# Performance work log

Measured on AMD Instinct MI355X. Metric: run time of the kernel, lower is better.

The kernel has to match this reference:

```python
import jax, jax.numpy as jnp
import numpy as np

NUM_HEAD = 16


def setup_inputs() -> dict:
    key = jax.random.key(0)
    k1, k2, k3 = jax.random.split(key, 3)
    E = 1024
    x = jax.random.normal(k1, (4, 2048, E), dtype=jnp.float32)
    W1 = jax.random.normal(k2, (E, 3 * E), dtype=jnp.float32) * 0.02
    b1 = jnp.zeros((3 * E,), dtype=jnp.float32)
    W2 = jax.random.normal(k3, (E, E), dtype=jnp.float32) * 0.02
    b2 = jnp.zeros((E,), dtype=jnp.float32)
    return {"x": x, "W1": W1, "b1": b1, "W2": W2, "b2": b2}


def reference(x, W1, b1, W2, b2):
    # Fused QKV projection: (n, s, 3E)
    h = x @ W1 + b1
    n, s, _ = h.shape
    # Split into heads FIRST (matches torch reshape), then transpose: (n, H, s, 3*d_head)
    h = h.reshape(n, s, NUM_HEAD, -1).transpose(0, 2, 1, 3)
    # Chunk last dim into q, k, v: each (n, H, s, d_head)
    q, k, v = jnp.split(h, 3, axis=-1)
    dk = jnp.asarray(v.shape[-1], x.dtype) ** 0.5
    # Naive full S x S attention (faithful to source)
    w = jnp.einsum("nhqd,nhkd->nhqk", q, k) / dk
    w = jax.nn.softmax(w, axis=-1)  # dropout1 is identity at eval
    att = jnp.einsum("nhqk,nhkd->nhqd", w, v)
    att = att.transpose(0, 2, 1, 3).reshape(n, s, -1)  # (n, s, E)
    return att @ W2 + b2  # dropout2 identity at eval
```

## Files before the change

kernel.cpp:

```cpp
#include <hip/hip_runtime.h>
#include <math.h>
#include <stdint.h>
#include <stddef.h>


#define SEQ    2048
#define NB     4
#define E_DIM  1024
#define N1     3072
#define M_TOK  8192
#define NHEAD  16
#define DHEAD  64

typedef __attribute__((ext_vector_type(4))) float    floatx4;
typedef __attribute__((ext_vector_type(8))) short    shortx8;
typedef __attribute__((ext_vector_type(4))) unsigned short ushortx4;

__device__ __forceinline__ unsigned short f2bf(float f) {
    union { float f; unsigned u; } v; v.f = f;
    unsigned r = (v.u + 0x7FFFu + ((v.u >> 16) & 1u)) >> 16;
    return (unsigned short)r;
}
__device__ __forceinline__ unsigned fbits(float f) {
    union { float f; unsigned u; } v; v.f = f; return v.u;
}
__device__ __forceinline__ float bitsf(unsigned u) {
    union { unsigned u; float f; } v; v.u = u; return v.f;
}

__device__ __forceinline__ void gl_lds16(const void* g, void* l) {
    __builtin_amdgcn_global_load_lds(
        (const __attribute__((address_space(1))) unsigned int*)g,
        (__attribute__((address_space(3))) unsigned int*)l, 16, 0, 0);
}

__global__ __launch_bounds__(256) void cvt_bf16(
    const float* __restrict__ in, unsigned short* __restrict__ out)
{
    const size_t i = ((size_t)blockIdx.x * 256 + threadIdx.x) * 8;
    float4 a = *(const float4*)(in + i);
    float4 b = *(const float4*)(in + i + 4);
    ushortx4 o0 = { f2bf(a.x), f2bf(a.y), f2bf(a.z), f2bf(a.w) };
    ushortx4 o1 = { f2bf(b.x), f2bf(b.y), f2bf(b.z), f2bf(b.w) };
    *(ushortx4*)(out + i)     = o0;
    *(ushortx4*)(out + i + 4) = o1;
}

__global__ __launch_bounds__(256) void cvt_transpose(
    const float* __restrict__ W, unsigned short* __restrict__ Wt, int K, int N)
{
    __shared__ unsigned short tile[32][33];
    const int tx = threadIdx.x, ty = threadIdx.y;
    const int n0 = blockIdx.x * 32, k0 = blockIdx.y * 32;
#pragma unroll
    for (int r = 0; r < 4; ++r) {
        const int k = ty + r * 8;
        tile[tx][k] = f2bf(W[(size_t)(k0 + k) * N + n0 + tx]);
    }
    __syncthreads();
#pragma unroll
    for (int r = 0; r < 4; ++r) {
        const int n = ty + r * 8;
        Wt[(size_t)(n0 + n) * K + k0 + tx] = tile[n][tx];
    }
}

__global__ __launch_bounds__(256) void vtrans(
    const unsigned short* __restrict__ h, unsigned short* __restrict__ Vt)
{
    __shared__ unsigned short tile[64][68];
    const int t  = threadIdx.x;
    const int bh = blockIdx.y, n = bh >> 4, head = bh & 15;
    const int s0 = blockIdx.x * 64;
    const unsigned short* hV = h + (size_t)n * SEQ * N1 + head * (3 * DHEAD) + 2 * DHEAD;

#pragma unroll
    for (int rr = 0; rr < 4; ++rr) {
        const int s  = rr * 16 + (t >> 4);
        const int d4 = (t & 15) * 4;
        ushortx4 v = *(const ushortx4*)(hV + (size_t)(s0 + s) * N1 + d4);
        tile[d4 + 0][s] = v.x;
        tile[d4 + 1][s] = v.y;
        tile[d4 + 2][s] = v.z;
        tile[d4 + 3][s] = v.w;
    }
    __syncthreads();
    unsigned short* Vb = Vt + (size_t)bh * DHEAD * SEQ;
#pragma unroll
    for (int rr = 0; rr < 4; ++rr) {
        const int d  = rr * 16 + (t >> 4);
        const int s4 = (t & 15) * 4;
        ushortx4 o = { tile[d][s4], tile[d][s4 + 1], tile[d][s4 + 2], tile[d][s4 + 3] };
        *(ushortx4*)(Vb + (size_t)d * SEQ + s0 + s4) = o;
    }
}

template <bool OUT_BF16>
__global__ __launch_bounds__(256) void gemm_bf16(
    const short* __restrict__ A, const short* __restrict__ Bt,
    const float* __restrict__ bias, void* __restrict__ Cout,
    int M, int N, int K)
{
    __shared__ short As[128 * 32];
    __shared__ short Bs[128 * 32];

    const int t    = threadIdx.x;
    const int lane = t & 63, w = t >> 6;
    const int quad = lane >> 4, l15 = lane & 15;
    const int bm = blockIdx.y * 128, bn = blockIdx.x * 128;
    const int m0w = (w >> 1) * 64, n0w = (w & 1) * 64;

    const int lrow = lane >> 2;
    const int lcol = (lane & 3) * 8;
    const short* Ag0 = A  + (size_t)(bm + (2 * w + 0) * 16 + lrow) * K + lcol;
    const short* Ag1 = A  + (size_t)(bm + (2 * w + 1) * 16 + lrow) * K + lcol;
    const short* Bg0 = Bt + (size_t)(bn + (2 * w + 0) * 16 + lrow) * K + lcol;
    const short* Bg1 = Bt + (size_t)(bn + (2 * w + 1) * 16 + lrow) * K + lcol;
    short* Al0 = As + (2 * w + 0) * 512;
    short* Al1 = As + (2 * w + 1) * 512;
    short* Bl0 = Bs + (2 * w + 0) * 512;
    short* Bl1 = Bs + (2 * w + 1) * 512;

    floatx4 acc[4][4];
#pragma unroll
    for (int i = 0; i < 4; ++i)
#pragma unroll
        for (int j = 0; j < 4; ++j) acc[i][j] = (floatx4)0.f;

    for (int k0 = 0; k0 < K; k0 += 32) {
        __syncthreads();
        gl_lds16(Ag0, Al0); gl_lds16(Ag1, Al1);
        gl_lds16(Bg0, Bl0); gl_lds16(Bg1, Bl1);
        Ag0 += 32; Ag1 += 32; Bg0 += 32; Bg1 += 32;
        __syncthreads();

        shortx8 af[4], bf[4];
#pragma unroll
        for (int mi = 0; mi < 4; ++mi)
            af[mi] = *(const shortx8*)(As + (m0w + mi * 16 + l15) * 32 + quad * 8);
#pragma unroll
        for (int ni = 0; ni < 4; ++ni)
            bf[ni] = *(const shortx8*)(Bs + (n0w + ni * 16 + l15) * 32 + quad * 8);
#pragma unroll
        for (int mi = 0; mi < 4; ++mi)
#pragma unroll
            for (int ni = 0; ni < 4; ++ni)
                acc[mi][ni] = __builtin_amdgcn_mfma_f32_16x16x32_bf16(
                    af[mi], bf[ni], acc[mi][ni], 0, 0, 0);
    }

    float bv[4];
#pragma unroll
    for (int ni = 0; ni < 4; ++ni) bv[ni] = bias[bn + n0w + ni * 16 + l15];

#pragma unroll
    for (int mi = 0; mi < 4; ++mi)
#pragma unroll
        for (int ni = 0; ni < 4; ++ni)
#pragma unroll
            for (int r = 0; r < 4; ++r) {
                const size_t row = bm + m0w + mi * 16 + quad * 4 + r;
                const size_t col = bn + n0w + ni * 16 + l15;
                const float  val = acc[mi][ni][r] + bv[ni];
                if (OUT_BF16)
                    ((unsigned short*)Cout)[row * N + col] = f2bf(val);
                else
                    ((float*)Cout)[row * N + col] = val;
            }
}

__global__ __launch_bounds__(256, 2) void attn_mfma(
    const short* __restrict__ h, const short* __restrict__ Vt,
    unsigned short* __restrict__ att)
{
    __shared__ short Ks[64 * 72];
    __shared__ short Vs[64 * 72];
    __shared__ short Pl[4][64 * 72];
    __shared__ float Ls[4][64];

    const int t    = threadIdx.x;
    const int lane = t & 63, w = t >> 6;
    const int quad = lane >> 4, l15 = lane & 15;
    const int bh = blockIdx.x, n = bh >> 4, head = bh & 15;
    const int q0 = blockIdx.y * 256 + w * 64;

    const short* hQ  = h + (size_t)n * SEQ * N1 + head * (3 * DHEAD);
    const short* hK  = hQ + DHEAD;
    const short* Vtb = Vt + (size_t)bh * DHEAD * SEQ;

    const int srow = t >> 2;
    const int scol = (t & 3) * 16;
    const short* gK = hK  + (size_t)srow * N1  + scol;
    const short* gV = Vtb + (size_t)srow * SEQ + scol;
    short* lK = Ks + srow * 72 + scol;
    short* lV = Vs + srow * 72 + scol;

    shortx8 qf[4][2];
#pragma unroll
    for (int qt = 0; qt < 4; ++qt)
#pragma unroll
        for (int kt = 0; kt < 2; ++kt)
            qf[qt][kt] = *(const shortx8*)(hQ + (size_t)(q0 + qt * 16 + l15) * N1
                                           + kt * 32 + quad * 8);

    floatx4 O[4][4];
    float lsum[4];
#pragma unroll
    for (int mi = 0; mi < 4; ++mi) {
        lsum[mi] = 0.f;
#pragma unroll
        for (int nt = 0; nt < 4; ++nt) O[mi][nt] = (floatx4)0.f;
    }

    int4 ka = *(const int4*)gK, kb = *(const int4*)(gK + 8);
    int4 va = *(const int4*)gV, vb = *(const int4*)(gV + 8);

    const float SC = 0.18033688f;
    short* Pw = Pl[w];

    for (int kv0 = 0; kv0 < SEQ; kv0 += 64) {
        __syncthreads();
        *(int4*)lK       = ka;
        *(int4*)(lK + 8) = kb;
        *(int4*)lV       = va;
        *(int4*)(lV + 8) = vb;
        __syncthreads();
        if (kv0 + 64 < SEQ) {
            const short* gKn = gK + (size_t)(kv0 + 64) * N1;
            const short* gVn = gV + (kv0 + 64);
            ka = *(const int4*)gKn; kb = *(const int4*)(gKn + 8);
            va = *(const int4*)gVn; vb = *(const int4*)(gVn + 8);
        }

#pragma unroll
        for (int kvt = 0; kvt < 4; ++kvt) {
            shortx8 kf0 = *(const shortx8*)(Ks + (kvt * 16 + l15) * 72 + quad * 8);
            shortx8 kf1 = *(const shortx8*)(Ks + (kvt * 16 + l15) * 72 + 32 + quad * 8);
            floatx4 s[4];
#pragma unroll
            for (int qt = 0; qt < 4; ++qt) {
                s[qt] = __builtin_amdgcn_mfma_f32_16x16x32_bf16(
                    kf0, qf[qt][0], (floatx4)0.f, 0, 0, 0);
                s[qt] = __builtin_amdgcn_mfma_f32_16x16x32_bf16(
                    kf1, qf[qt][1], s[qt], 0, 0, 0);
            }
#pragma unroll
            for (int qt = 0; qt < 4; ++qt) {
                const float p0 = exp2f(s[qt][0] * SC);
                const float p1 = exp2f(s[qt][1] * SC);
                const float p2 = exp2f(s[qt][2] * SC);
                const float p3 = exp2f(s[qt][3] * SC);
                const unsigned d01 = __builtin_amdgcn_perm(fbits(p1), fbits(p0), 0x07060302u);
                const unsigned d23 = __builtin_amdgcn_perm(fbits(p3), fbits(p2), 0x07060302u);
                lsum[qt] += bitsf(d01 << 16) + bitsf(d01 & 0xFFFF0000u)
                          + bitsf(d23 << 16) + bitsf(d23 & 0xFFFF0000u);
                uint2 pk = { d01, d23 };
                *(uint2*)(Pw + (qt * 16 + l15) * 72 + kvt * 16 + quad * 4) = pk;
            }
        }

#pragma unroll
        for (int kt2 = 0; kt2 < 2; ++kt2) {
            shortx8 pf[4], vf[4];
#pragma unroll
            for (int mi = 0; mi < 4; ++mi)
                pf[mi] = *(const shortx8*)(Pw + (mi * 16 + l15) * 72 + kt2 * 32 + quad * 8);
#pragma unroll
            for (int nt = 0; nt < 4; ++nt)
                vf[nt] = *(const shortx8*)(Vs + (nt * 16 + l15) * 72 + kt2 * 32 + quad * 8);
#pragma unroll
            for (int mi = 0; mi < 4; ++mi)
#pragma unroll
                for (int nt = 0; nt < 4; ++nt)
                    O[mi][nt] = __builtin_amdgcn_mfma_f32_16x16x32_bf16(
                        pf[mi], vf[nt], O[mi][nt], 0, 0, 0);
        }
    }

#pragma unroll
    for (int qt = 0; qt < 4; ++qt) {
        lsum[qt] += __shfl_xor(lsum[qt], 16);
        lsum[qt] += __shfl_xor(lsum[qt], 32);
    }
    if (quad == 0) {
#pragma unroll
        for (int qt = 0; qt < 4; ++qt) Ls[w][qt * 16 + l15] = lsum[qt];
    }

#pragma unroll
    for (int mi = 0; mi < 4; ++mi)
#pragma unroll
        for (int r = 0; r < 4; ++r) {
            const int   ql  = mi * 16 + quad * 4 + r;
            const float inv = 1.f / Ls[w][ql];
            const size_t row = (size_t)n * SEQ + q0 + ql;
#pragma unroll
            for (int nt = 0; nt < 4; ++nt)
                att[row * E_DIM + head * DHEAD + nt * 16 + l15] =
                    f2bf(O[mi][nt][r] * inv);
        }
}

extern "C" void kernel_launch(void* const* d_in, const int* in_sizes, int n_in,
                              void* d_out, int out_size, void* d_ws, size_t ws_size,
                              hipStream_t stream)
{
    const float* x  = (const float*)d_in[0];
    const float* W1 = (const float*)d_in[1];
    const float* b1 = (const float*)d_in[2];
    const float* W2 = (const float*)d_in[3];
    const float* b2 = (const float*)d_in[4];
    float* out = (float*)d_out;

    char* ws = (char*)d_ws;
    unsigned short* x_bf  = (unsigned short*)(ws);
    unsigned short* W1t   = (unsigned short*)(ws + (16u << 20));
    unsigned short* W2t   = (unsigned short*)(ws + (22u << 20));
    unsigned short* h_bf  = (unsigned short*)(ws + (24u << 20));
    unsigned short* attb  = (unsigned short*)(ws + (72u << 20));
    unsigned short* Vtw   = (unsigned short*)(ws + (88u << 20));

    cvt_bf16<<<dim3((M_TOK * E_DIM) / (256 * 8)), 256, 0, stream>>>(x, x_bf);
    cvt_transpose<<<dim3(N1 / 32, E_DIM / 32), dim3(32, 8), 0, stream>>>(W1, W1t, E_DIM, N1);
    cvt_transpose<<<dim3(E_DIM / 32, E_DIM / 32), dim3(32, 8), 0, stream>>>(W2, W2t, E_DIM, E_DIM);

    gemm_bf16<true><<<dim3(N1 / 128, M_TOK / 128), 256, 0, stream>>>(
        (const short*)x_bf, (const short*)W1t, b1, h_bf, M_TOK, N1, E_DIM);

    vtrans<<<dim3(SEQ / 64, NB * NHEAD), 256, 0, stream>>>(h_bf, Vtw);

    attn_mfma<<<dim3(NB * NHEAD, SEQ / 256), 256, 0, stream>>>(
        (const short*)h_bf, (const short*)Vtw, attb);

    gemm_bf16<false><<<dim3(E_DIM / 128, M_TOK / 128), 256, 0, stream>>>(
        (const short*)attb, (const short*)W2t, b2, out, M_TOK, E_DIM, E_DIM);
}
```

Before: 327.1 us.

## Fuse V transpose into QKV GEMM epilogue, swizzle attention LDS, prescale Q

```diff
diff --git a/kernel.cpp b/kernel.cpp
--- a/kernel.cpp
+++ b/kernel.cpp
@@ -65,40 +65,11 @@
     }
 }
 
-__global__ __launch_bounds__(256) void vtrans(
-    const unsigned short* __restrict__ h, unsigned short* __restrict__ Vt)
-{
-    __shared__ unsigned short tile[64][68];
-    const int t  = threadIdx.x;
-    const int bh = blockIdx.y, n = bh >> 4, head = bh & 15;
-    const int s0 = blockIdx.x * 64;
-    const unsigned short* hV = h + (size_t)n * SEQ * N1 + head * (3 * DHEAD) + 2 * DHEAD;
-
-#pragma unroll
-    for (int rr = 0; rr < 4; ++rr) {
-        const int s  = rr * 16 + (t >> 4);
-        const int d4 = (t & 15) * 4;
-        ushortx4 v = *(const ushortx4*)(hV + (size_t)(s0 + s) * N1 + d4);
-        tile[d4 + 0][s] = v.x;
-        tile[d4 + 1][s] = v.y;
-        tile[d4 + 2][s] = v.z;
-        tile[d4 + 3][s] = v.w;
-    }
-    __syncthreads();
-    unsigned short* Vb = Vt + (size_t)bh * DHEAD * SEQ;
-#pragma unroll
-    for (int rr = 0; rr < 4; ++rr) {
-        const int d  = rr * 16 + (t >> 4);
-        const int s4 = (t & 15) * 4;
-        ushortx4 o = { tile[d][s4], tile[d][s4 + 1], tile[d][s4 + 2], tile[d][s4 + 3] };
-        *(ushortx4*)(Vb + (size_t)d * SEQ + s0 + s4) = o;
-    }
-}
-
-template <bool OUT_BF16>
+template <bool OUT_BF16, bool FUSE>
 __global__ __launch_bounds__(256) void gemm_bf16(
     const short* __restrict__ A, const short* __restrict__ Bt,
     const float* __restrict__ bias, void* __restrict__ Cout,
+    unsigned short* __restrict__ Vt,
     int M, int N, int K)
 {
     __shared__ short As[128 * 32];
@@ -154,33 +125,55 @@
     for (int ni = 0; ni < 4; ++ni) bv[ni] = bias[bn + n0w + ni * 16 + l15];
 
 #pragma unroll
-    for (int mi = 0; mi < 4; ++mi)
-#pragma unroll
-        for (int ni = 0; ni < 4; ++ni)
-#pragma unroll
-            for (int r = 0; r < 4; ++r) {
-                const size_t row = bm + m0w + mi * 16 + quad * 4 + r;
-                const size_t col = bn + n0w + ni * 16 + l15;
-                const float  val = acc[mi][ni][r] + bv[ni];
-                if (OUT_BF16)
-                    ((unsigned short*)Cout)[row * N + col] = f2bf(val);
-                else
-                    ((float*)Cout)[row * N + col] = val;
+    for (int ni = 0; ni < 4; ++ni) {
+        const int col   = bn + n0w + ni * 16 + l15;
+        const int cm    = col % 192;
+        const int vhead = col / 192;
+#pragma unroll
+        for (int mi = 0; mi < 4; ++mi) {
+            const int row0 = bm + m0w + mi * 16 + quad * 4;
+            float v[4];
+#pragma unroll
+            for (int r = 0; r < 4; ++r) v[r] = acc[mi][ni][r] + bv[ni];
+            if (OUT_BF16) {
+                if (FUSE && cm < DHEAD) {
+#pragma unroll
+                    for (int r = 0; r < 4; ++r) v[r] *= 0.125f;
+                }
+                unsigned short* H = (unsigned short*)Cout;
+#pragma unroll
+                for (int r = 0; r < 4; ++r)
+                    H[(size_t)(row0 + r) * N + col] = f2bf(v[r]);
+                if (FUSE && cm >= 2 * DHEAD) {
+                    const int nb = row0 >> 11;
+                    const int s  = row0 & 2047;
+                    const int d  = cm - 2 * DHEAD;
+                    ushortx4 pk = { f2bf(v[0]), f2bf(v[1]), f2bf(v[2]), f2bf(v[3]) };
+                    *(ushortx4*)(Vt + ((size_t)(nb * NHEAD + vhead) * DHEAD + d) * SEQ + s) = pk;
+                }
+            } else {
+                float* C = (float*)Cout;
+#pragma unroll
+                for (int r = 0; r < 4; ++r)
+                    C[(size_t)(row0 + r) * N + col] = v[r];
             }
-}
-
-__global__ __launch_bounds__(256, 2) void attn_mfma(
+        }
+    }
+}
+
+__global__ __launch_bounds__(256, 3) void attn_mfma(
     const short* __restrict__ h, const short* __restrict__ Vt,
     unsigned short* __restrict__ att)
 {
-    __shared__ short Ks[64 * 72];
-    __shared__ short Vs[64 * 72];
-    __shared__ short Pl[4][64 * 72];
+    __shared__ short Ks[64 * 64];
+    __shared__ short Vs[64 * 64];
+    __shared__ short Pl[4][64 * 64];
     __shared__ float Ls[4][64];
 
     const int t    = threadIdx.x;
     const int lane = t & 63, w = t >> 6;
     const int quad = lane >> 4, l15 = lane & 15;
+    const int r7   = l15 & 7;
     const int bh = blockIdx.x, n = bh >> 4, head = bh & 15;
     const int q0 = blockIdx.y * 256 + w * 64;
 
@@ -189,11 +182,14 @@
     const short* Vtb = Vt + (size_t)bh * DHEAD * SEQ;
 
     const int srow = t >> 2;
-    const int scol = (t & 3) * 16;
-    const short* gK = hK  + (size_t)srow * N1  + scol;
-    const short* gV = Vtb + (size_t)srow * SEQ + scol;
-    short* lK = Ks + srow * 72 + scol;
-    short* lV = Vs + srow * 72 + scol;
+    const int sc0  = (t & 3) * 2;
+    const int sk   = srow & 7;
+    const short* gK = hK  + (size_t)srow * N1  + sc0 * 8;
+    const short* gV = Vtb + (size_t)srow * SEQ + sc0 * 8;
+    short* lK0 = Ks + srow * 64 + ((sc0    ) ^ sk) * 8;
+    short* lK1 = Ks + srow * 64 + ((sc0 + 1) ^ sk) * 8;
+    short* lV0 = Vs + srow * 64 + ((sc0    ) ^ sk) * 8;
+    short* lV1 = Vs + srow * 64 + ((sc0 + 1) ^ sk) * 8;
 
     shortx8 qf[4][2];
 #pragma unroll
@@ -215,15 +211,14 @@
     int4 ka = *(const int4*)gK, kb = *(const int4*)(gK + 8);
     int4 va = *(const int4*)gV, vb = *(const int4*)(gV + 8);
 
-    const float SC = 0.18033688f;
     short* Pw = Pl[w];
 
     for (int kv0 = 0; kv0 < SEQ; kv0 += 64) {
         __syncthreads();
-        *(int4*)lK       = ka;
-        *(int4*)(lK + 8) = kb;
-        *(int4*)lV       = va;
-        *(int4*)(lV + 8) = vb;
+        *(int4*)lK0 = ka;
+        *(int4*)lK1 = kb;
+        *(int4*)lV0 = va;
+        *(int4*)lV1 = vb;
         __syncthreads();
         if (kv0 + 64 < SEQ) {
             const short* gKn = gK + (size_t)(kv0 + 64) * N1;
@@ -234,8 +229,9 @@
 
 #pragma unroll
         for (int kvt = 0; kvt < 4; ++kvt) {
-            shortx8 kf0 = *(const shortx8*)(Ks + (kvt * 16 + l15) * 72 + quad * 8);
-            shortx8 kf1 = *(const shortx8*)(Ks + (kvt * 16 + l15) * 72 + 32 + quad * 8);
+            const short* krow = Ks + (kvt * 16 + l15) * 64;
+            shortx8 kf0 = *(const shortx8*)(krow + ((quad ^ r7) * 8));
+            shortx8 kf1 = *(const shortx8*)(krow + (((quad ^ r7) ^ 4) * 8));
             floatx4 s[4];
 #pragma unroll
             for (int qt = 0; qt < 4; ++qt) {
@@ -246,28 +242,31 @@
             }
 #pragma unroll
             for (int qt = 0; qt < 4; ++qt) {
-                const float p0 = exp2f(s[qt][0] * SC);
-                const float p1 = exp2f(s[qt][1] * SC);
-                const float p2 = exp2f(s[qt][2] * SC);
-                const float p3 = exp2f(s[qt][3] * SC);
+                const float p0 = __expf(s[qt][0]);
+                const float p1 = __expf(s[qt][1]);
+                const float p2 = __expf(s[qt][2]);
+                const float p3 = __expf(s[qt][3]);
                 const unsigned d01 = __builtin_amdgcn_perm(fbits(p1), fbits(p0), 0x07060302u);
                 const unsigned d23 = __builtin_amdgcn_perm(fbits(p3), fbits(p2), 0x07060302u);
                 lsum[qt] += bitsf(d01 << 16) + bitsf(d01 & 0xFFFF0000u)
                           + bitsf(d23 << 16) + bitsf(d23 & 0xFFFF0000u);
                 uint2 pk = { d01, d23 };
-                *(uint2*)(Pw + (qt * 16 + l15) * 72 + kvt * 16 + quad * 4) = pk;
+                *(uint2*)(Pw + (qt * 16 + l15) * 64
+                          + ((2 * kvt + (quad >> 1)) ^ r7) * 8 + (quad & 1) * 4) = pk;
             }
         }
 
 #pragma unroll
         for (int kt2 = 0; kt2 < 2; ++kt2) {
+            const int coff = (((kt2 * 4 + quad) ^ r7)) * 8;
             shortx8 pf[4], vf[4];
 #pragma unroll
             for (int mi = 0; mi < 4; ++mi)
-                pf[mi] = *(const shortx8*)(Pw + (mi * 16 + l15) * 72 + kt2 * 32 + quad * 8);
+                pf[mi] = *(const shortx8*)(Pw + (mi * 16 + l15) * 64 +
+                                           (((kt2 * 4 + quad) ^ r7)) * 8);
 #pragma unroll
             for (int nt = 0; nt < 4; ++nt)
-                vf[nt] = *(const shortx8*)(Vs + (nt * 16 + l15) * 72 + kt2 * 32 + quad * 8);
+                vf[nt] = *(const shortx8*)(Vs + (nt * 16 + l15) * 64 + coff);
 #pragma unroll
             for (int mi = 0; mi < 4; ++mi)
 #pragma unroll
@@ -324,14 +323,12 @@
     cvt_transpose<<<dim3(N1 / 32, E_DIM / 32), dim3(32, 8), 0, stream>>>(W1, W1t, E_DIM, N1);
     cvt_transpose<<<dim3(E_DIM / 32, E_DIM / 32), dim3(32, 8), 0, stream>>>(W2, W2t, E_DIM, E_DIM);
 
-    gemm_bf16<true><<<dim3(N1 / 128, M_TOK / 128), 256, 0, stream>>>(
-        (const short*)x_bf, (const short*)W1t, b1, h_bf, M_TOK, N1, E_DIM);
-
-    vtrans<<<dim3(SEQ / 64, NB * NHEAD), 256, 0, stream>>>(h_bf, Vtw);
+    gemm_bf16<true, true><<<dim3(N1 / 128, M_TOK / 128), 256, 0, stream>>>(
+        (const short*)x_bf, (const short*)W1t, b1, h_bf, Vtw, M_TOK, N1, E_DIM);
 
     attn_mfma<<<dim3(NB * NHEAD, SEQ / 256), 256, 0, stream>>>(
         (const short*)h_bf, (const short*)Vtw, attb);
 
-    gemm_bf16<false><<<dim3(E_DIM / 128, M_TOK / 128), 256, 0, stream>>>(
-        (const short*)attb, (const short*)W2t, b2, out, M_TOK, E_DIM, E_DIM);
-}
+    gemm_bf16<false, false><<<dim3(E_DIM / 128, M_TOK / 128), 256, 0, stream>>>(
+        (const short*)attb, (const short*)W2t, b2, out, nullptr, M_TOK, E_DIM, E_DIM);
+}
```

After: 301.3 us. -7.9%, faster.
